# Optimization experiments

Hardware: AMD Instinct MI355X
Metric: run time of the kernel (lower is better)

## Reference

```python
import jax, jax.numpy as jnp
import numpy as np

LN_EPS = 1e-3

def setup_inputs() -> dict:
    key = jax.random.key(0)
    ks = jax.random.split(key, 3)
    B, H, W, C = 32, 64, 48, 256
    groups = 8
    d = C // groups
    x = jax.random.normal(ks[0], (B, H, W, C), dtype=jnp.float32)
    conv1x1_w = jax.random.normal(ks[1], (d, d), dtype=jnp.float32) * (1.0 / np.sqrt(d))
    conv1x1_b = jnp.zeros((d,), dtype=jnp.float32)
    conv3x3_w = jax.random.normal(ks[2], (3, 3, d, d), dtype=jnp.float32) * (1.0 / np.sqrt(9 * d))
    conv3x3_b = jnp.zeros((d,), dtype=jnp.float32)
    ln_gamma = jnp.ones((d,), dtype=jnp.float32)
    ln_beta = jnp.zeros((d,), dtype=jnp.float32)
    return {"x": x, "conv1x1_w": conv1x1_w, "conv1x1_b": conv1x1_b,
            "conv3x3_w": conv3x3_w, "conv3x3_b": conv3x3_b,
            "ln_gamma": ln_gamma, "ln_beta": ln_beta, "groups": groups}


def reference(x, conv1x1_w, conv1x1_b, conv3x3_w, conv3x3_b, ln_gamma, ln_beta, groups):
    B, H, W, C = x.shape
    g = groups
    d = C // g
    # group split: [B,H,W,C] -> [B*g, H, W, d]
    gx = x.reshape(B, H, W, g, d).transpose(0, 3, 1, 2, 4).reshape(B * g, H, W, d)
    # adaptive pools to (H,1) and (1,W) == mean over W / mean over H
    x_h = gx.mean(axis=2, keepdims=True)                 # [Bg,H,1,d]
    x_w = gx.mean(axis=1, keepdims=True)                 # [Bg,1,W,d]
    hw = jnp.concatenate([x_h, x_w.transpose(0, 2, 1, 3)], axis=1)  # [Bg,H+W,1,d]
    # conv1x1 == per-position linear over channels
    hw = jnp.einsum('bhwd,de->bhwe', hw, conv1x1_w) + conv1x1_b
    xh = jax.nn.sigmoid(hw[:, :H])                       # [Bg,H,1,d]
    xw = jax.nn.sigmoid(hw[:, H:].transpose(0, 2, 1, 3)) # [Bg,1,W,d]
    # LayerNorm over last axis
    y = gx * xh * xw
    mu = y.mean(axis=-1, keepdims=True)
    var = jnp.mean(jnp.square(y - mu), axis=-1, keepdims=True)
    x1 = (y - mu) * jax.lax.rsqrt(var + LN_EPS) * ln_gamma + ln_beta
    # conv3x3 SAME on grouped features
    x2 = jax.lax.conv_general_dilated(
        gx, conv3x3_w, window_strides=(1, 1), padding='SAME',
        dimension_numbers=('NHWC', 'HWIO', 'NHWC')) + conv3x3_b
    # channel softmax of GAP, cross matmuls -> spatial gate
    x11 = jax.nn.softmax(x1.mean(axis=(1, 2)), axis=-1)  # [Bg,d]
    x21 = jax.nn.softmax(x2.mean(axis=(1, 2)), axis=-1)  # [Bg,d]
    w1 = jnp.einsum('bd,bhwd->bhw', x11, x2)
    w2 = jnp.einsum('bd,bhwd->bhw', x21, x1)
    gate = jax.nn.sigmoid((w1 + w2)[..., None])          # [Bg,H,W,1]
    out = gx * gate
    out = out.reshape(B, g, H, W, d).transpose(0, 2, 3, 1, 4).reshape(B, H, W, C)
    return out
```

## Files before the change

kernel.cpp:

```cpp
#include <hip/hip_runtime.h>
#include <math.h>

#define B_ 32
#define H_ 64
#define W_ 48
#define C_ 256
#define G_ 8
#define D_ 32
#define BG_ (B_*G_)
#define LN_EPS_ 1e-3f
#define NPIX_ (H_*W_)
#define SROWB 3072

typedef short bf16x8 __attribute__((ext_vector_type(8)));
typedef float f32x4 __attribute__((ext_vector_type(4)));

__device__ __forceinline__ float sigmoidf_(float v) { return 1.0f / (1.0f + expf(-v)); }

__device__ __forceinline__ unsigned short f2bf(float f) {
    unsigned u = __float_as_uint(f);
    u = u + 0x7fffu + ((u >> 16) & 1u);
    return (unsigned short)(u >> 16);
}
__device__ __forceinline__ float bflo(unsigned u) { return __uint_as_float(u << 16); }
__device__ __forceinline__ float bfhi(unsigned u) { return __uint_as_float(u & 0xffff0000u); }

__device__ __forceinline__ int swz16(int px, int slot) {
    return ((px << 6) + (slot << 4)) ^ ((px & 7) << 4);
}

__global__ __launch_bounds__(256) void k0_prep(const float* __restrict__ w3,
                                               unsigned short* __restrict__ wbf)
{
    int i = blockIdx.x * 256 + threadIdx.x;
    if (i < 9 * D_ * D_) {
        int t = i >> 10;
        int rem = i & 1023;
        int e = rem >> 5, d = rem & 31;
        wbf[i] = f2bf(w3[((t << 5) + d) * D_ + e]);
    }
}

__global__ __launch_bounds__(512) void k1_means(const float* __restrict__ x,
                                                const float* __restrict__ w1,
                                                const float* __restrict__ b1,
                                                const float* __restrict__ w3,
                                                const float* __restrict__ b3,
                                                const float* __restrict__ gamma,
                                                const float* __restrict__ beta,
                                                unsigned short* __restrict__ xhb,
                                                unsigned short* __restrict__ xwb,
                                                float* __restrict__ s1,
                                                float* __restrict__ s2)
{
    __shared__ float mh[H_][D_];
    __shared__ float mwp[8][W_][D_];
    __shared__ float wls[D_ * D_];
    __shared__ float xhf[H_][D_];
    __shared__ float xwf[W_][36];
    __shared__ float cst[4][D_];
    __shared__ float Tg[D_];
    __shared__ float Sl[9][D_];
    __shared__ float S2p[9][D_];
    __shared__ float s1red[8][D_];

    int bg = blockIdx.x;
    int b = bg >> 3, gi = bg & 7;
    const float* base = x + (size_t)b * H_ * W_ * C_ + gi * D_;
    int t = threadIdx.x;
    int lane = t & 63;
    int wv = t >> 6;
    int c4 = lane & 7;
    int pxg = lane >> 3;

    for (int i = t; i < D_ * D_; i += 512) wls[i] = w1[i];

    float4 colp[6];
    #pragma unroll
    for (int j = 0; j < 6; ++j) colp[j] = make_float4(0.f, 0.f, 0.f, 0.f);

    for (int i = 0; i < 8; i += 2) {
        int ha = (wv << 3) + i;
        int hb = ha + 1;
        const float* rowa = base + (size_t)ha * W_ * C_;
        const float* rowb = base + (size_t)hb * W_ * C_;
        float4 va[6], vb[6];
        #pragma unroll
        for (int j = 0; j < 6; ++j) {
            va[j] = *(const float4*)(rowa + (size_t)(pxg + 8 * j) * C_ + (c4 << 2));
            vb[j] = *(const float4*)(rowb + (size_t)(pxg + 8 * j) * C_ + (c4 << 2));
        }
        float4 rpa = make_float4(0.f, 0.f, 0.f, 0.f);
        float4 rpb = make_float4(0.f, 0.f, 0.f, 0.f);
        #pragma unroll
        for (int j = 0; j < 6; ++j) {
            float4 v = va[j];
            colp[j].x += v.x; colp[j].y += v.y; colp[j].z += v.z; colp[j].w += v.w;
            rpa.x += v.x; rpa.y += v.y; rpa.z += v.z; rpa.w += v.w;
            float4 u = vb[j];
            colp[j].x += u.x; colp[j].y += u.y; colp[j].z += u.z; colp[j].w += u.w;
            rpb.x += u.x; rpb.y += u.y; rpb.z += u.z; rpb.w += u.w;
        }
        #pragma unroll
        for (int s = 8; s <= 32; s <<= 1) {
            rpa.x += __shfl_xor(rpa.x, s); rpa.y += __shfl_xor(rpa.y, s);
            rpa.z += __shfl_xor(rpa.z, s); rpa.w += __shfl_xor(rpa.w, s);
            rpb.x += __shfl_xor(rpb.x, s); rpb.y += __shfl_xor(rpb.y, s);
            rpb.z += __shfl_xor(rpb.z, s); rpb.w += __shfl_xor(rpb.w, s);
        }
        if (lane < 8) {
            *(float4*)&mh[ha][c4 << 2] = rpa;
            *(float4*)&mh[hb][c4 << 2] = rpb;
        }
    }
    #pragma unroll
    for (int j = 0; j < 6; ++j)
        *(float4*)&mwp[wv][pxg + 8 * j][c4 << 2] = colp[j];
    __syncthreads();

    for (int i = t; i < W_ * D_; i += 512) {
        int px = i >> 5, c = i & 31;
        float s = 0.f;
        #pragma unroll
        for (int v = 0; v < 8; ++v) s += mwp[v][px][c];
        mwp[0][px][c] = s;
    }
    if (t < 128) {
        int k = t >> 5, c = t & 31;
        int hh = (k >> 1) ? (H_ - 1) : 0;
        int ww = (k & 1) ? (W_ - 1) : 0;
        cst[k][c] = base[(size_t)(hh * W_ + ww) * C_ + c];
    }
    __syncthreads();

    if (t < 32) {
        float s = 0.f;
        for (int h = 0; h < H_; ++h) s += mh[h][t];
        Tg[t] = s;
    }
    for (int i = t; i < (H_ + W_) * D_; i += 512) {
        int pos = i >> 5, e = i & 31;
        const float* m = (pos < H_) ? mh[pos] : mwp[0][pos - H_];
        float scale = (pos < H_) ? (1.0f / W_) : (1.0f / H_);
        float dot = 0.f;
        #pragma unroll
        for (int d = 0; d < D_; ++d) dot += m[d] * wls[d * D_ + e];
        float sg = sigmoidf_(b1[e] + dot * scale);
        if (pos < H_) { xhf[pos][e] = sg; xhb[(((size_t)bg << 6) + pos) * D_ + e] = f2bf(sg); }
        else { xwf[pos - H_][e] = sg; xwb[((size_t)bg * W_ + (pos - H_)) * D_ + e] = f2bf(sg); }
    }
    __syncthreads();

    if (t < 288) {
        int tap = t >> 5, d = t & 31;
        int dh = tap / 3, dw = tap % 3;
        float S = Tg[d];
        if (dh == 0) S -= mh[H_ - 1][d];
        else if (dh == 2) S -= mh[0][d];
        if (dw == 0) S -= mwp[0][W_ - 1][d];
        else if (dw == 2) S -= mwp[0][0][d];
        if (dh != 1 && dw != 1) S += cst[(dh == 0 ? 2 : 0) + (dw == 0 ? 1 : 0)][d];
        Sl[tap][d] = S;
    }
    __syncthreads();
    if (t < 288) {
        int tap = t >> 5, e = t & 31;
        float a = 0.f;
        #pragma unroll
        for (int d = 0; d < D_; ++d) a += w3[((tap << 5) + d) * D_ + e] * Sl[tap][d];
        S2p[tap][e] = a;
    }
    __syncthreads();
    if (t < 32) {
        float a = (float)NPIX_ * b3[t];
        #pragma unroll
        for (int tap = 0; tap < 9; ++tap) a += S2p[tap][t];
        s2[bg * D_ + t] = a;
    }

    float s1p[32];
    #pragma unroll
    for (int c = 0; c < 32; ++c) s1p[c] = 0.f;
    #pragma unroll
    for (int k = 0; k < 6; ++k) {
        int p = t + (k << 9);
        int h = p / W_;
        int w = p - h * W_;
        const float4* vp = (const float4*)(base + (size_t)(h * W_ + w) * C_);
        float y[32];
        float mu = 0.f;
        #pragma unroll
        for (int j = 0; j < 8; ++j) {
            float4 v = vp[j];
            float4 a = *(const float4*)&xhf[h][j << 2];
            float4 bw = *(const float4*)&xwf[w][j << 2];
            y[4 * j + 0] = v.x * a.x * bw.x;
            y[4 * j + 1] = v.y * a.y * bw.y;
            y[4 * j + 2] = v.z * a.z * bw.z;
            y[4 * j + 3] = v.w * a.w * bw.w;
            mu += y[4 * j + 0] + y[4 * j + 1] + y[4 * j + 2] + y[4 * j + 3];
        }
        mu *= (1.0f / D_);
        float var = 0.f;
        #pragma unroll
        for (int c = 0; c < 32; ++c) { float dl = y[c] - mu; var += dl * dl; }
        var *= (1.0f / D_);
        float rs = rsqrtf(var + LN_EPS_);
        #pragma unroll
        for (int j = 0; j < 8; ++j) {
            float4 gq = ((const float4*)gamma)[j];
            float4 bt = ((const float4*)beta)[j];
            s1p[4 * j + 0] += (y[4 * j + 0] - mu) * rs * gq.x + bt.x;
            s1p[4 * j + 1] += (y[4 * j + 1] - mu) * rs * gq.y + bt.y;
            s1p[4 * j + 2] += (y[4 * j + 2] - mu) * rs * gq.z + bt.z;
            s1p[4 * j + 3] += (y[4 * j + 3] - mu) * rs * gq.w + bt.w;
        }
    }
    #pragma unroll
    for (int c = 0; c < 32; ++c) {
        float vv = s1p[c];
        vv += __shfl_xor(vv, 1);  vv += __shfl_xor(vv, 2);  vv += __shfl_xor(vv, 4);
        vv += __shfl_xor(vv, 8);  vv += __shfl_xor(vv, 16); vv += __shfl_xor(vv, 32);
        s1p[c] = vv;
    }
    if (lane == 0) {
        #pragma unroll
        for (int c = 0; c < 32; ++c) s1red[wv][c] = s1p[c];
    }
    __syncthreads();
    if (t < 32) {
        float a = 0.f;
        #pragma unroll
        for (int v = 0; v < 8; ++v) a += s1red[v][t];
        s1[bg * D_ + t] = a;
    }
}

__global__ __launch_bounds__(64) void k4_softmax(const float* __restrict__ s1,
                                                 const float* __restrict__ s2,
                                                 float* __restrict__ x11,
                                                 float* __restrict__ x21)
{
    int bg = blockIdx.x;
    int lane = threadIdx.x;
    const float* s = (lane < 32) ? s1 : s2;
    float* o = (lane < 32) ? x11 : x21;
    int c = lane & 31;
    float v = s[bg * D_ + c] * (1.0f / (float)NPIX_);
    float m = v;
    m = fmaxf(m, __shfl_xor(m, 1));  m = fmaxf(m, __shfl_xor(m, 2));
    m = fmaxf(m, __shfl_xor(m, 4));  m = fmaxf(m, __shfl_xor(m, 8));
    m = fmaxf(m, __shfl_xor(m, 16));
    float e = expf(v - m);
    float sm = e;
    sm += __shfl_xor(sm, 1);  sm += __shfl_xor(sm, 2);
    sm += __shfl_xor(sm, 4);  sm += __shfl_xor(sm, 8);
    sm += __shfl_xor(sm, 16);
    o[bg * D_ + c] = e / sm;
}

__global__ __launch_bounds__(256) void k5_conv(const float* __restrict__ x,
                                               const unsigned short* __restrict__ wbf,
                                               const float* __restrict__ b3,
                                               const unsigned short* __restrict__ xhb,
                                               const unsigned short* __restrict__ xwb,
                                               const float* __restrict__ gamma,
                                               const float* __restrict__ beta,
                                               const float* __restrict__ x11,
                                               const float* __restrict__ x21,
                                               float* __restrict__ out)
{
    __shared__ unsigned short sbuf[10 * W_ * D_];
    __shared__ float wbuf[8][W_];
    int bi = blockIdx.x;
    int bg = bi >> 3;
    int h0 = (bi & 7) << 3;
    int b = bg >> 3, gi = bg & 7;
    const float* base = x + (size_t)b * H_ * W_ * C_ + gi * D_;
    int t = threadIdx.x;
    int lane = t & 63;
    int wv = t >> 6;
    const int e0 = lane & 15;
    const int ko = (lane >> 4) << 3;

    bf16x8 wf[9][2];
    #pragma unroll
    for (int tp = 0; tp < 9; ++tp)
        #pragma unroll
        for (int n = 0; n < 2; ++n)
            wf[tp][n] = *(const bf16x8*)(const void*)(wbf + (((tp << 5) + (n << 4) + e0) << 5) + ko);
    float be0 = b3[e0], be1 = b3[e0 + 16];
    float a110 = x11[bg * D_ + e0], a111 = x11[bg * D_ + e0 + 16];

    #pragma unroll
    for (int kk = 0; kk < 15; ++kk) {
        int i = t + (kk << 8);
        int r = i / 384;
        int rem = i - r * 384;
        int w = rem >> 3, cc = rem & 7;
        int hh = h0 - 1 + r;
        unsigned u0 = 0, u1 = 0;
        if (hh >= 0 && hh < H_) {
            float4 v = *(const float4*)(base + (size_t)(hh * W_ + w) * C_ + (cc << 2));
            u0 = (unsigned)f2bf(v.x) | ((unsigned)f2bf(v.y) << 16);
            u1 = (unsigned)f2bf(v.z) | ((unsigned)f2bf(v.w) << 16);
        }
        int addr = r * SROWB + ((((w << 6) + (cc << 3))) ^ ((w & 7) << 4));
        *(uint2*)((char*)sbuf + addr) = make_uint2(u0, u1);
    }
    __syncthreads();

    int swz9[9]; bool inv9[9];
    #pragma unroll
    for (int m = 0; m < 3; ++m)
        #pragma unroll
        for (int dw = 0; dw < 3; ++dw) {
            int pxi = (m << 4) + e0 + dw - 1;
            int pxc = pxi < 0 ? 0 : (pxi > 47 ? 47 : pxi);
            swz9[m * 3 + dw] = swz16(pxc, lane >> 4);
            inv9[m * 3 + dw] = (pxi != pxc);
        }
    const bf16x8 z8 = {0, 0, 0, 0, 0, 0, 0, 0};

    for (int q = 0; q < 2; ++q) {
        int r = (wv << 1) + q;
        #pragma unroll
        for (int m = 0; m < 3; ++m) {
            f32x4 acc0 = {be0, be0, be0, be0};
            f32x4 acc1 = {be1, be1, be1, be1};
            #pragma unroll
            for (int dh = 0; dh < 3; ++dh) {
                int srowB = (r + dh) * SROWB;
                #pragma unroll
                for (int dw = 0; dw < 3; ++dw) {
                    bf16x8 a = *(const bf16x8*)(const void*)((const char*)sbuf + srowB + swz9[m * 3 + dw]);
                    if ((m == 0 && dw == 0) || (m == 2 && dw == 2)) {
                        if (inv9[m * 3 + dw]) a = z8;
                    }
                    acc0 = __builtin_amdgcn_mfma_f32_16x16x32_bf16(a, wf[dh * 3 + dw][0], acc0, 0, 0, 0);
                    acc1 = __builtin_amdgcn_mfma_f32_16x16x32_bf16(a, wf[dh * 3 + dw][1], acc1, 0, 0, 0);
                }
            }
            #pragma unroll
            for (int rg = 0; rg < 4; ++rg) {
                float p = a110 * acc0[rg] + a111 * acc1[rg];
                p += __shfl_xor(p, 1); p += __shfl_xor(p, 2);
                p += __shfl_xor(p, 4); p += __shfl_xor(p, 8);
                if (e0 == 0) wbuf[r][(m << 4) + ((lane >> 4) << 2) + rg] = p;
            }
        }
    }
    __syncthreads();

    for (int p = t; p < 8 * W_; p += 256) {
        int r = p / W_;
        int w = p - r * W_;
        int h = h0 + r;
        int srowB = (r + 1) * SROWB;
        const uint4* ph4 = (const uint4*)(xhb + (((size_t)bg << 6) + h) * D_);
        const uint4* pw4 = (const uint4*)(xwb + ((size_t)bg * W_ + w) * D_);
        float y[32];
        float mu = 0.f;
        #pragma unroll
        for (int j = 0; j < 4; ++j) {
            uint4 uv = *(const uint4*)((const char*)sbuf + srowB + swz16(w, j));
            uint4 uh = ph4[j];
            uint4 uw = pw4[j];
            float vv[8], ah[8], aw[8];
            vv[0]=bflo(uv.x); vv[1]=bfhi(uv.x); vv[2]=bflo(uv.y); vv[3]=bfhi(uv.y);
            vv[4]=bflo(uv.z); vv[5]=bfhi(uv.z); vv[6]=bflo(uv.w); vv[7]=bfhi(uv.w);
            ah[0]=bflo(uh.x); ah[1]=bfhi(uh.x); ah[2]=bflo(uh.y); ah[3]=bfhi(uh.y);
            ah[4]=bflo(uh.z); ah[5]=bfhi(uh.z); ah[6]=bflo(uh.w); ah[7]=bfhi(uh.w);
            aw[0]=bflo(uw.x); aw[1]=bfhi(uw.x); aw[2]=bflo(uw.y); aw[3]=bfhi(uw.y);
            aw[4]=bflo(uw.z); aw[5]=bfhi(uw.z); aw[6]=bflo(uw.w); aw[7]=bfhi(uw.w);
            #pragma unroll
            for (int kk = 0; kk < 8; ++kk) {
                float yy = vv[kk] * ah[kk] * aw[kk];
                y[j * 8 + kk] = yy;
                mu += yy;
            }
        }
        mu *= (1.0f / D_);
        float var = 0.f;
        #pragma unroll
        for (int c = 0; c < D_; ++c) { float dl = y[c] - mu; var += dl * dl; }
        var *= (1.0f / D_);
        float rs = rsqrtf(var + LN_EPS_);

        float w2 = 0.f;
        #pragma unroll
        for (int c = 0; c < D_; ++c) {
            float x1v = (y[c] - mu) * rs * gamma[c] + beta[c];
            w2 += x21[bg * D_ + c] * x1v;
        }
        float gate = sigmoidf_(wbuf[r][w] + w2);

        const float4* vp = (const float4*)(base + (size_t)(h * W_ + w) * C_);
        float4* op = (float4*)(out + (size_t)b * H_ * W_ * C_ + (size_t)(h * W_ + w) * C_ + gi * D_);
        #pragma unroll
        for (int j = 0; j < 8; ++j) {
            float4 vv = vp[j];
            float4 tq;
            tq.x = vv.x * gate; tq.y = vv.y * gate;
            tq.z = vv.z * gate; tq.w = vv.w * gate;
            op[j] = tq;
        }
    }
}

extern "C" void kernel_launch(void* const* d_in, const int* in_sizes, int n_in,
                              void* d_out, int out_size, void* d_ws, size_t ws_size,
                              hipStream_t stream)
{
    const float* x     = (const float*)d_in[0];
    const float* w1    = (const float*)d_in[1];
    const float* b1    = (const float*)d_in[2];
    const float* w3    = (const float*)d_in[3];
    const float* b3    = (const float*)d_in[4];
    const float* gamma = (const float*)d_in[5];
    const float* beta  = (const float*)d_in[6];

    char* wsb = (char*)d_ws;
    unsigned short* xhb = (unsigned short*)wsb;
    unsigned short* xwb = (unsigned short*)(wsb + 1048576);
    float* s1  = (float*)(wsb + 1835008);
    float* s2  = (float*)(wsb + 1867776);
    float* x11 = (float*)(wsb + 1900544);
    float* x21 = (float*)(wsb + 1933312);
    unsigned short* wbf = (unsigned short*)(wsb + 1966080);

    k0_prep<<<36, 256, 0, stream>>>(w3, wbf);
    k1_means<<<BG_, 512, 0, stream>>>(x, w1, b1, w3, b3, gamma, beta, xhb, xwb, s1, s2);
    k4_softmax<<<BG_, 64, 0, stream>>>(s1, s2, x11, x21);
    k5_conv<<<BG_ * 8, 256, 0, stream>>>(x, wbf, b3, xhb, xwb, gamma, beta, x11, x21,
                                         (float*)d_out);
}
```

Measured before the change: 292.6 us.

## Split LN-sum pass into separate kernel and enlarge conv tiles to 16 rows

Moves the LayerNorm channel-sum pass out of the per-group means kernel into a new kernel with four blocks per group that accumulates with atomics into a zeroed buffer. This raises parallelism, since the old kernel ran only 256 blocks. The conv kernel now handles 16 rows per 512-thread block, which cuts halo overhead, and it reuses the bf16 values from shared memory for the output instead of re-reading x. The cost is an extra full pass over x, a memset, atomics, and output computed from bf16-rounded x, which lowers precision.

```diff
diff --git a/kernel.cpp b/kernel.cpp
--- a/kernel.cpp
+++ b/kernel.cpp
@@ -41,28 +41,22 @@
     }
 }
 
-__global__ __launch_bounds__(512) void k1_means(const float* __restrict__ x,
-                                                const float* __restrict__ w1,
-                                                const float* __restrict__ b1,
-                                                const float* __restrict__ w3,
-                                                const float* __restrict__ b3,
-                                                const float* __restrict__ gamma,
-                                                const float* __restrict__ beta,
-                                                unsigned short* __restrict__ xhb,
-                                                unsigned short* __restrict__ xwb,
-                                                float* __restrict__ s1,
-                                                float* __restrict__ s2)
+__global__ __launch_bounds__(512) void k1_sums(const float* __restrict__ x,
+                                               const float* __restrict__ w1,
+                                               const float* __restrict__ b1,
+                                               const float* __restrict__ w3,
+                                               const float* __restrict__ b3,
+                                               unsigned short* __restrict__ xhb,
+                                               unsigned short* __restrict__ xwb,
+                                               float* __restrict__ s2)
 {
     __shared__ float mh[H_][D_];
     __shared__ float mwp[8][W_][D_];
     __shared__ float wls[D_ * D_];
-    __shared__ float xhf[H_][D_];
-    __shared__ float xwf[W_][36];
     __shared__ float cst[4][D_];
     __shared__ float Tg[D_];
     __shared__ float Sl[9][D_];
     __shared__ float S2p[9][D_];
-    __shared__ float s1red[8][D_];
 
     int bg = blockIdx.x;
     int b = bg >> 3, gi = bg & 7;
@@ -146,8 +140,8 @@
         #pragma unroll
         for (int d = 0; d < D_; ++d) dot += m[d] * wls[d * D_ + e];
         float sg = sigmoidf_(b1[e] + dot * scale);
-        if (pos < H_) { xhf[pos][e] = sg; xhb[(((size_t)bg << 6) + pos) * D_ + e] = f2bf(sg); }
-        else { xwf[pos - H_][e] = sg; xwb[((size_t)bg * W_ + (pos - H_)) * D_ + e] = f2bf(sg); }
+        if (pos < H_) xhb[(((size_t)bg << 6) + pos) * D_ + e] = f2bf(sg);
+        else          xwb[((size_t)bg * W_ + (pos - H_)) * D_ + e] = f2bf(sg);
     }
     __syncthreads();
 
@@ -177,28 +171,57 @@
         for (int tap = 0; tap < 9; ++tap) a += S2p[tap][t];
         s2[bg * D_ + t] = a;
     }
+}
+
+__global__ __launch_bounds__(256) void k2_s1(const float* __restrict__ x,
+                                             const unsigned short* __restrict__ xhb,
+                                             const unsigned short* __restrict__ xwb,
+                                             const float* __restrict__ gamma,
+                                             const float* __restrict__ beta,
+                                             float* __restrict__ s1)
+{
+    __shared__ float red[4][D_];
+    int bi = blockIdx.x;
+    int bg = bi >> 2;
+    int h0 = (bi & 3) << 4;
+    int b = bg >> 3, gi = bg & 7;
+    const float* base = x + (size_t)b * H_ * W_ * C_ + gi * D_;
+    int t = threadIdx.x;
+    int lane = t & 63;
+    int wv = t >> 6;
 
     float s1p[32];
     #pragma unroll
     for (int c = 0; c < 32; ++c) s1p[c] = 0.f;
-    #pragma unroll
-    for (int k = 0; k < 6; ++k) {
-        int p = t + (k << 9);
-        int h = p / W_;
-        int w = p - h * W_;
+
+    #pragma unroll
+    for (int k = 0; k < 3; ++k) {
+        int p = t + (k << 8);
+        int r = p / W_;
+        int w = p - r * W_;
+        int h = h0 + r;
         const float4* vp = (const float4*)(base + (size_t)(h * W_ + w) * C_);
+        const uint4* ph4 = (const uint4*)(xhb + (((size_t)bg << 6) + h) * D_);
+        const uint4* pw4 = (const uint4*)(xwb + ((size_t)bg * W_ + w) * D_);
         float y[32];
         float mu = 0.f;
         #pragma unroll
-        for (int j = 0; j < 8; ++j) {
-            float4 v = vp[j];
-            float4 a = *(const float4*)&xhf[h][j << 2];
-            float4 bw = *(const float4*)&xwf[w][j << 2];
-            y[4 * j + 0] = v.x * a.x * bw.x;
-            y[4 * j + 1] = v.y * a.y * bw.y;
-            y[4 * j + 2] = v.z * a.z * bw.z;
-            y[4 * j + 3] = v.w * a.w * bw.w;
-            mu += y[4 * j + 0] + y[4 * j + 1] + y[4 * j + 2] + y[4 * j + 3];
+        for (int j = 0; j < 4; ++j) {
+            float4 v0 = vp[2 * j], v1 = vp[2 * j + 1];
+            uint4 uh = ph4[j];
+            uint4 uw = pw4[j];
+            float vv[8] = {v0.x, v0.y, v0.z, v0.w, v1.x, v1.y, v1.z, v1.w};
+            float ah[8], aw[8];
+            ah[0]=bflo(uh.x); ah[1]=bfhi(uh.x); ah[2]=bflo(uh.y); ah[3]=bfhi(uh.y);
+            ah[4]=bflo(uh.z); ah[5]=bfhi(uh.z); ah[6]=bflo(uh.w); ah[7]=bfhi(uh.w);
+            aw[0]=bflo(uw.x); aw[1]=bfhi(uw.x); aw[2]=bflo(uw.y); aw[3]=bfhi(uw.y);
+            aw[4]=bflo(uw.z); aw[5]=bfhi(uw.z); aw[6]=bflo(uw.w); aw[7]=bfhi(uw.w);
+            #pragma unroll
+            for (int kk = 0; kk < 8; ++kk) {
+                float yy = vv[kk] * ah[kk] * aw[kk];
+                y[j * 8 + kk] = yy;
+                mu += yy;
+            }
         }
         mu *= (1.0f / D_);
         float var = 0.f;
@@ -225,14 +248,12 @@
     }
     if (lane == 0) {
         #pragma unroll
-        for (int c = 0; c < 32; ++c) s1red[wv][c] = s1p[c];
+        for (int c = 0; c < 32; ++c) red[wv][c] = s1p[c];
     }
     __syncthreads();
     if (t < 32) {
-        float a = 0.f;
-        #pragma unroll
-        for (int v = 0; v < 8; ++v) a += s1red[v][t];
-        s1[bg * D_ + t] = a;
+        float a = red[0][t] + red[1][t] + red[2][t] + red[3][t];
+        atomicAdd(&s1[bg * D_ + t], a);
     }
 }
 
@@ -259,7 +280,7 @@
     o[bg * D_ + c] = e / sm;
 }
 
-__global__ __launch_bounds__(256) void k5_conv(const float* __restrict__ x,
+__global__ __launch_bounds__(512) void k5_conv(const float* __restrict__ x,
                                                const unsigned short* __restrict__ wbf,
                                                const float* __restrict__ b3,
                                                const unsigned short* __restrict__ xhb,
@@ -270,11 +291,11 @@
                                                const float* __restrict__ x21,
                                                float* __restrict__ out)
 {
-    __shared__ unsigned short sbuf[10 * W_ * D_];
-    __shared__ float wbuf[8][W_];
+    __shared__ unsigned short sbuf[18 * W_ * D_];
+    __shared__ float wbuf[16][W_];
     int bi = blockIdx.x;
-    int bg = bi >> 3;
-    int h0 = (bi & 7) << 3;
+    int bg = bi >> 2;
+    int h0 = (bi & 3) << 4;
     int b = bg >> 3, gi = bg & 7;
     const float* base = x + (size_t)b * H_ * W_ * C_ + gi * D_;
     int t = threadIdx.x;
@@ -293,20 +314,22 @@
     float a110 = x11[bg * D_ + e0], a111 = x11[bg * D_ + e0 + 16];
 
     #pragma unroll
-    for (int kk = 0; kk < 15; ++kk) {
-        int i = t + (kk << 8);
-        int r = i / 384;
-        int rem = i - r * 384;
-        int w = rem >> 3, cc = rem & 7;
-        int hh = h0 - 1 + r;
-        unsigned u0 = 0, u1 = 0;
-        if (hh >= 0 && hh < H_) {
-            float4 v = *(const float4*)(base + (size_t)(hh * W_ + w) * C_ + (cc << 2));
-            u0 = (unsigned)f2bf(v.x) | ((unsigned)f2bf(v.y) << 16);
-            u1 = (unsigned)f2bf(v.z) | ((unsigned)f2bf(v.w) << 16);
-        }
-        int addr = r * SROWB + ((((w << 6) + (cc << 3))) ^ ((w & 7) << 4));
-        *(uint2*)((char*)sbuf + addr) = make_uint2(u0, u1);
+    for (int kk = 0; kk < 14; ++kk) {
+        int i = t + (kk << 9);
+        if (i < 6912) {
+            int r = i / 384;
+            int rem = i - r * 384;
+            int w = rem >> 3, cc = rem & 7;
+            int hh = h0 - 1 + r;
+            unsigned u0 = 0, u1 = 0;
+            if (hh >= 0 && hh < H_) {
+                float4 v = *(const float4*)(base + (size_t)(hh * W_ + w) * C_ + (cc << 2));
+                u0 = (unsigned)f2bf(v.x) | ((unsigned)f2bf(v.y) << 16);
+                u1 = (unsigned)f2bf(v.z) | ((unsigned)f2bf(v.w) << 16);
+            }
+            int addr = r * SROWB + ((((w << 6) + (cc << 3))) ^ ((w & 7) << 4));
+            *(uint2*)((char*)sbuf + addr) = make_uint2(u0, u1);
+        }
     }
     __syncthreads();
 
@@ -352,30 +375,30 @@
     }
     __syncthreads();
 
-    for (int p = t; p < 8 * W_; p += 256) {
+    for (int p = t; p < 16 * W_; p += 512) {
         int r = p / W_;
         int w = p - r * W_;
         int h = h0 + r;
         int srowB = (r + 1) * SROWB;
         const uint4* ph4 = (const uint4*)(xhb + (((size_t)bg << 6) + h) * D_);
         const uint4* pw4 = (const uint4*)(xwb + ((size_t)bg * W_ + w) * D_);
-        float y[32];
+        float v[32], y[32];
         float mu = 0.f;
         #pragma unroll
         for (int j = 0; j < 4; ++j) {
             uint4 uv = *(const uint4*)((const char*)sbuf + srowB + swz16(w, j));
             uint4 uh = ph4[j];
             uint4 uw = pw4[j];
-            float vv[8], ah[8], aw[8];
-            vv[0]=bflo(uv.x); vv[1]=bfhi(uv.x); vv[2]=bflo(uv.y); vv[3]=bfhi(uv.y);
-            vv[4]=bflo(uv.z); vv[5]=bfhi(uv.z); vv[6]=bflo(uv.w); vv[7]=bfhi(uv.w);
+            float ah[8], aw[8];
+            v[j*8+0]=bflo(uv.x); v[j*8+1]=bfhi(uv.x); v[j*8+2]=bflo(uv.y); v[j*8+3]=bfhi(uv.y);
+            v[j*8+4]=bflo(uv.z); v[j*8+5]=bfhi(uv.z); v[j*8+6]=bflo(uv.w); v[j*8+7]=bfhi(uv.w);
             ah[0]=bflo(uh.x); ah[1]=bfhi(uh.x); ah[2]=bflo(uh.y); ah[3]=bfhi(uh.y);
             ah[4]=bflo(uh.z); ah[5]=bfhi(uh.z); ah[6]=bflo(uh.w); ah[7]=bfhi(uh.w);
             aw[0]=bflo(uw.x); aw[1]=bfhi(uw.x); aw[2]=bflo(uw.y); aw[3]=bfhi(uw.y);
             aw[4]=bflo(uw.z); aw[5]=bfhi(uw.z); aw[6]=bflo(uw.w); aw[7]=bfhi(uw.w);
             #pragma unroll
             for (int kk = 0; kk < 8; ++kk) {
-                float yy = vv[kk] * ah[kk] * aw[kk];
+                float yy = v[j * 8 + kk] * ah[kk] * aw[kk];
                 y[j * 8 + kk] = yy;
                 mu += yy;
             }
@@ -395,14 +418,12 @@
         }
         float gate = sigmoidf_(wbuf[r][w] + w2);
 
-        const float4* vp = (const float4*)(base + (size_t)(h * W_ + w) * C_);
         float4* op = (float4*)(out + (size_t)b * H_ * W_ * C_ + (size_t)(h * W_ + w) * C_ + gi * D_);
         #pragma unroll
         for (int j = 0; j < 8; ++j) {
-            float4 vv = vp[j];
             float4 tq;
-            tq.x = vv.x * gate; tq.y = vv.y * gate;
-            tq.z = vv.z * gate; tq.w = vv.w * gate;
+            tq.x = v[4 * j + 0] * gate; tq.y = v[4 * j + 1] * gate;
+            tq.z = v[4 * j + 2] * gate; tq.w = v[4 * j + 3] * gate;
             op[j] = tq;
         }
     }
@@ -429,9 +450,12 @@
     float* x21 = (float*)(wsb + 1933312);
     unsigned short* wbf = (unsigned short*)(wsb + 1966080);
 
+    hipMemsetAsync(s1, 0, 32768, stream);
+
     k0_prep<<<36, 256, 0, stream>>>(w3, wbf);
-    k1_means<<<BG_, 512, 0, stream>>>(x, w1, b1, w3, b3, gamma, beta, xhb, xwb, s1, s2);
+    k1_sums<<<BG_, 512, 0, stream>>>(x, w1, b1, w3, b3, xhb, xwb, s2);
+    k2_s1<<<BG_ * 4, 256, 0, stream>>>(x, xhb, xwb, gamma, beta, s1);
     k4_softmax<<<BG_, 64, 0, stream>>>(s1, s2, x11, x21);
-    k5_conv<<<BG_ * 8, 256, 0, stream>>>(x, wbf, b3, xhb, xwb, gamma, beta, x11, x21,
+    k5_conv<<<BG_ * 4, 512, 0, stream>>>(x, wbf, b3, xhb, xwb, gamma, beta, x11, x21,
                                          (float*)d_out);
 }
```

After: 300.1 us. 1.03x slower.
